# Kernel tuning notes

Hardware: AMD Instinct MI355X
Metric: run time of the kernel (lower is better)

The kernel has to match this reference:

```python
import jax, jax.numpy as jnp
import numpy as np
import math

MODEL_DIM = 1024
HEAD_DIM = 64
NUM_HEADS = 16
FF_MULT = 4
FF_DIM = FF_MULT * MODEL_DIM
ATTN_DIM = NUM_HEADS * HEAD_DIM
FUSED_DIMS = (ATTN_DIM, ATTN_DIM, ATTN_DIM, FF_DIM, FF_DIM)


def setup_inputs() -> dict:
    key = jax.random.key(0)
    k_x, k_in, k_attn, k_ff = jax.random.split(key, 4)
    B, S = 2, 2048
    inputs = jax.random.normal(k_x, (B, S, MODEL_DIM), dtype=jnp.float32)
    # LayerNorm affine params (torch defaults: weight=1, bias=0)
    ln_w = jnp.ones((MODEL_DIM,), dtype=jnp.float32)
    ln_b = jnp.zeros((MODEL_DIM,), dtype=jnp.float32)
    # Linear weights stored as [in, out] (equivalent to torch W.T)
    s_in = 1.0 / math.sqrt(MODEL_DIM)
    w_in = jax.random.uniform(k_in, (MODEL_DIM, sum(FUSED_DIMS)), jnp.float32, -s_in, s_in)
    s_a = 1.0 / math.sqrt(ATTN_DIM)
    w_attn = jax.random.uniform(k_attn, (ATTN_DIM, MODEL_DIM), jnp.float32, -s_a, s_a)
    s_f = 1.0 / math.sqrt(FF_DIM)
    w_ff = jax.random.uniform(k_ff, (FF_DIM, MODEL_DIM), jnp.float32, -s_f, s_f)
    return {"inputs": inputs, "ln_w": ln_w, "ln_b": ln_b,
            "w_in": w_in, "w_attn": w_attn, "w_ff": w_ff}


def _layer_norm(x, w, b, eps=1e-5):
    mu = jnp.mean(x, axis=-1, keepdims=True)
    var = jnp.var(x, axis=-1, keepdims=True)
    return (x - mu) * jax.lax.rsqrt(var + eps) * w + b


def reference(inputs, ln_w, ln_b, w_in, w_attn, w_ff):
    B, S, D = inputs.shape
    units = _layer_norm(inputs, ln_w, ln_b)
    proj = units @ w_in                                   # [B,S,3*A+2*F]
    splits = np.cumsum(FUSED_DIMS)[:-1]
    q, k, v, ff, ff_gate = jnp.split(proj, splits, axis=-1)
    # split heads: [B,S,H*d] -> [B,H,S,d]
    def heads(t):
        return t.reshape(B, S, NUM_HEADS, HEAD_DIM).transpose(0, 2, 1, 3)
    q, k, v = heads(q), heads(k), heads(v)
    scale = 1.0 / math.sqrt(HEAD_DIM)
    score = jnp.einsum('bhsd,bhTd->bhsT', q, k) * scale   # [B,H,S,S]
    weight = jax.nn.softmax(score, axis=-1)
    attn = jnp.einsum('bhsT,bhTd->bhsd', weight, v)       # [B,H,S,d]
    concat = attn.transpose(0, 2, 1, 3).reshape(B, S, ATTN_DIM)
    attn_out = concat @ w_attn                            # [B,S,D]
    ff_out = (ff * jax.nn.gelu(ff_gate, approximate=True)) @ w_ff
    return inputs + attn_out + ff_out
```

## Files before the change

kernel.cpp:

```cpp
#include <hip/hip_runtime.h>
#include <hip/hip_bf16.h>
#include <cstdint>
#include <cstddef>

typedef __bf16 bf16;
typedef __bf16 bf16x8 __attribute__((ext_vector_type(8)));
typedef float f32x4 __attribute__((ext_vector_type(4)));

#define MFMA16(a, b, c) __builtin_amdgcn_mfma_f32_16x16x32_bf16(a, b, c, 0, 0, 0)

#define GLOBAL_LOAD_LDS16(gptr, lptr)                                          \
  __builtin_amdgcn_global_load_lds(                                            \
      (const __attribute__((address_space(1))) void*)(gptr),                   \
      (__attribute__((address_space(3))) void*)(lptr), 16, 0, 0)

__global__ __launch_bounds__(256) void prep(const float* __restrict__ w_in,
                                            const float* __restrict__ w_attn,
                                            const float* __restrict__ w_ff,
                                            bf16* __restrict__ wt_in,
                                            bf16* __restrict__ wtcat,
                                            const float* __restrict__ x,
                                            const float* __restrict__ ln_w,
                                            const float* __restrict__ ln_b,
                                            bf16* __restrict__ xn) {
  __shared__ __align__(16) char sm[4352];
  if (blockIdx.x < 16384) {
    float(*t)[33] = (float(*)[33])sm;
    int id = blockIdx.x;
    const float* src; bf16* dst;
    int srcN, srccol0, LDO, mode, obase, goff, kcol0, ntn;
    if (id < 3072) {
      src = w_in; dst = wt_in; srcN = 11264; srccol0 = 0; LDO = 1024;
      mode = 0; obase = 0; goff = 0; kcol0 = 0; ntn = 96;
    } else if (id < 7168) {
      id -= 3072; src = w_in; dst = wt_in; srcN = 11264; srccol0 = 3072;
      LDO = 1024; mode = 1; obase = 3072; goff = 0; kcol0 = 0; ntn = 128;
    } else if (id < 11264) {
      id -= 7168; src = w_in; dst = wt_in; srcN = 11264; srccol0 = 7168;
      LDO = 1024; mode = 1; obase = 3072; goff = 64; kcol0 = 0; ntn = 128;
    } else if (id < 12288) {
      id -= 11264; src = w_attn; dst = wtcat; srcN = 1024; srccol0 = 0;
      LDO = 5120; mode = 0; obase = 0; goff = 0; kcol0 = 0; ntn = 32;
    } else {
      id -= 12288; src = w_ff; dst = wtcat; srcN = 1024; srccol0 = 0;
      LDO = 5120; mode = 0; obase = 0; goff = 0; kcol0 = 1024; ntn = 32;
    }
    const int n0 = (id % ntn) * 32, k0 = (id / ntn) * 32;
    const int tx = threadIdx.x & 31, ty = threadIdx.x >> 5;
    for (int i = ty; i < 32; i += 8)
      t[i][tx] = src[(size_t)(k0 + i) * srcN + srccol0 + n0 + tx];
    __syncthreads();
    for (int i = ty; i < 32; i += 8) {
      int n = n0 + i;
      int orow = mode ? (obase + ((n >> 6) << 7) + goff + (n & 63)) : (obase + n);
      dst[(size_t)orow * LDO + kcol0 + k0 + tx] = (bf16)t[tx][i];
    }
  } else {
    float* rs = (float*)sm;
    float* rss = rs + 256;
    const int row = blockIdx.x - 16384;
    const int tid = threadIdx.x;
    const float* xr = x + (size_t)row * 1024;
    float4 v = *(const float4*)&xr[tid * 4];
    float s = v.x + v.y + v.z + v.w;
    float ss = v.x * v.x + v.y * v.y + v.z * v.z + v.w * v.w;
    rs[tid] = s; rss[tid] = ss;
    __syncthreads();
    for (int off = 128; off > 0; off >>= 1) {
      if (tid < off) { rs[tid] += rs[tid + off]; rss[tid] += rss[tid + off]; }
      __syncthreads();
    }
    const float mean = rs[0] * (1.f / 1024.f);
    const float var = rss[0] * (1.f / 1024.f) - mean * mean;
    const float rstd = rsqrtf(var + 1e-5f);
    const float* vp = (const float*)&v;
    for (int i = 0; i < 4; i++) {
      int c = tid * 4 + i;
      xn[(size_t)row * 1024 + c] = (bf16)((vp[i] - mean) * rstd * ln_w[c] + ln_b[c]);
    }
  }
}

__global__ __launch_bounds__(256) void vtrans(const bf16* __restrict__ proj,
                                              bf16* __restrict__ vt) {
  __shared__ bf16 t[64][80];
  const int tid = threadIdx.x;
  const int s0 = blockIdx.x * 64;
  const int h = blockIdx.y, b = blockIdx.z;
  constexpr size_t LDP = 3072;
  const bf16* src = proj + (size_t)b * 2048 * LDP + 2048 + h * 64;
  {
    int s = tid >> 2, d0 = (tid & 3) * 16;
    *(bf16x8*)&t[s][d0]     = *(const bf16x8*)&src[(size_t)(s0 + s) * LDP + d0];
    *(bf16x8*)&t[s][d0 + 8] = *(const bf16x8*)&src[(size_t)(s0 + s) * LDP + d0 + 8];
  }
  __syncthreads();
  {
    int d = tid >> 2, sb = (tid & 3) * 16;
    bf16* dst = vt + ((size_t)(b * 16 + h) * 64 + d) * 2048 + s0 + sb;
    bf16x8 o0, o1;
    for (int i = 0; i < 8; i++) { o0[i] = t[sb + i][d]; o1[i] = t[sb + 8 + i][d]; }
    *(bf16x8*)&dst[0] = o0;
    *(bf16x8*)&dst[8] = o1;
  }
}

__global__ __launch_bounds__(256) void flash_attn(const bf16* __restrict__ proj,
                                                  const bf16* __restrict__ vt,
                                                  bf16* __restrict__ hcat) {
  __shared__ __align__(16) char smem[50176];
  bf16* Ks = (bf16*)smem;
  bf16* Vs = (bf16*)(smem + 16384);
  bf16* Ps = (bf16*)(smem + 32768);
  const int tid = threadIdx.x;
  const int wave = tid >> 6, lane = tid & 63;
  const int quad = lane >> 4, l16 = lane & 15;
  const int q0 = blockIdx.x * 64;
  const int h = blockIdx.y, b = blockIdx.z;
  constexpr size_t LDP = 3072;
  const bf16* Qb = proj + (size_t)b * 2048 * LDP + h * 64;
  const bf16* Kb = proj + (size_t)b * 2048 * LDP + 1024 + h * 64;
  const bf16* Vt = vt + (size_t)(b * 16 + h) * 64 * 2048;

  const int qrow = q0 + wave * 16 + l16;
  bf16x8 aq0r = *(const bf16x8*)&Qb[(size_t)qrow * LDP + quad * 8];
  bf16x8 aq1r = *(const bf16x8*)&Qb[(size_t)qrow * LDP + 32 + quad * 8];
  bf16x8 aq0, aq1;
#pragma unroll
  for (int i = 0; i < 8; i++) {
    aq0[i] = (bf16)((float)aq0r[i] * 0.125f);
    aq1[i] = (bf16)((float)aq1r[i] * 0.125f);
  }

  f32x4 O[4] = {};
  float plrow[4] = {0.f, 0.f, 0.f, 0.f};

  const int krow_ = wave * 8 + (lane >> 3);
  const int kq_ = ((lane & 7) ^ (krow_ & 7)) * 8;
  const int vrow_ = wave * 4 + (lane >> 4);
  const int vq_ = ((lane & 15) ^ (vrow_ & 15)) * 8;

  for (int j0 = 0; j0 < 2048; j0 += 128) {
#pragma unroll
    for (int p = 0; p < 4; p++) {
      int kr = p * 32 + krow_;
      GLOBAL_LOAD_LDS16(&Kb[(size_t)(j0 + kr) * LDP + kq_],
                        &Ks[kr * 64 + (lane & 7) * 8]);
      int vr = p * 16 + vrow_;
      GLOBAL_LOAD_LDS16(&Vt[(size_t)vr * 2048 + j0 + vq_],
                        &Vs[vr * 128 + (lane & 15) * 8]);
    }
    __syncthreads();

    f32x4 sa[8];
#pragma unroll
    for (int nt = 0; nt < 8; nt++) {
      int r = nt * 16 + l16;
      bf16x8 bk0 = *(const bf16x8*)&Ks[r * 64 + (quad ^ (r & 7)) * 8];
      bf16x8 bk1 = *(const bf16x8*)&Ks[r * 64 + ((quad + 4) ^ (r & 7)) * 8];
      f32x4 t = {};
      t = MFMA16(aq0, bk0, t);
      sa[nt] = MFMA16(aq1, bk1, t);
    }

    bf16* Pw = Ps + wave * (16 * 136);
#pragma unroll
    for (int r = 0; r < 4; r++) {
      bf16* pr = &Pw[(quad * 4 + r) * 136];
      float ts = 0.f;
#pragma unroll
      for (int nt = 0; nt < 8; nt++) {
        float p = __expf(sa[nt][r]);
        pr[nt * 16 + l16] = (bf16)p;
        ts += p;
      }
      plrow[r] += ts;
    }

#pragma unroll
    for (int kg = 0; kg < 4; kg++) {
      bf16x8 aP = *(const bf16x8*)&Pw[l16 * 136 + kg * 32 + quad * 8];
#pragma unroll
      for (int nb = 0; nb < 4; nb++) {
        int vrr = nb * 16 + l16;
        int vsl = ((kg * 4 + quad) ^ (vrr & 15)) * 8;
        bf16x8 bv = *(const bf16x8*)&Vs[vrr * 128 + vsl];
        O[nb] = MFMA16(aP, bv, O[nb]);
      }
    }
    __syncthreads();
  }

#pragma unroll
  for (int r = 0; r < 4; r++) {
    float ts = plrow[r];
#pragma unroll
    for (int d = 1; d < 16; d <<= 1) ts += __shfl_xor(ts, d, 64);
    float inv = 1.f / ts;
    size_t row = (size_t)b * 2048 + q0 + wave * 16 + quad * 4 + r;
#pragma unroll
    for (int nb = 0; nb < 4; nb++)
      hcat[row * 5120 + h * 64 + nb * 16 + l16] = (bf16)(O[nb][r] * inv);
  }
}

__global__ __launch_bounds__(512, 2) void gemm_proj(const bf16* __restrict__ A,
                                                    const bf16* __restrict__ Bt,
                                                    bf16* __restrict__ proj,
                                                    bf16* __restrict__ hcat) {
  constexpr int K = 1024, NT = 32;
  __shared__ __align__(16) char smem[98304];
  const int tid = threadIdx.x;
  const int wave = tid >> 6, lane = tid & 63;
  const int quad = lane >> 4, l16 = lane & 15;
  const int wm0 = (wave >> 2) * 128, wn0 = (wave & 3) * 64;
  const size_t rowA0 = (size_t)blockIdx.y * 256;
  const size_t rowB0 = (size_t)blockIdx.x * 256;
  const bf16* Ag = A + rowA0 * K;
  const bf16* Bg = Bt + rowB0 * K;

  const int srow = tid >> 2;
  const int sslot = tid & 3;
  const int rslot = (quad ^ ((l16 >> 1) & 3)) * 8;

  f32x4 acc[8][4] = {};

  auto STAGE = [&](int kt, int buf) {
    bf16* As = (bf16*)(smem + buf * 32768);
    bf16* Bs = As + 256 * 32;
    const int k0 = kt * 32;
#pragma unroll
    for (int p = 0; p < 2; p++) {
      int r = p * 128 + srow;
      int kq = (sslot ^ ((r >> 1) & 3)) * 8;
      GLOBAL_LOAD_LDS16(&Ag[(size_t)r * K + k0 + kq], &As[r * 32 + sslot * 8]);
      GLOBAL_LOAD_LDS16(&Bg[(size_t)r * K + k0 + kq], &Bs[r * 32 + sslot * 8]);
    }
  };

  STAGE(0, 0);
  STAGE(1, 1);
  asm volatile("s_waitcnt vmcnt(4)" ::: "memory");
  __builtin_amdgcn_s_barrier();
  asm volatile("" ::: "memory");

  int cbuf = 0, sbuf = 2;
#pragma unroll 1
  for (int kt = 0; kt < NT; kt++) {
    if (kt + 2 < NT) STAGE(kt + 2, sbuf);
    const bf16* As = (const bf16*)(smem + cbuf * 32768);
    const bf16* Bs = As + 256 * 32;
    bf16x8 bfr[4];
#pragma unroll
    for (int j = 0; j < 4; j++)
      bfr[j] = *(const bf16x8*)&Bs[(wn0 + j * 16 + l16) * 32 + rslot];
#pragma unroll
    for (int ih = 0; ih < 2; ih++) {
      bf16x8 af[4];
#pragma unroll
      for (int i = 0; i < 4; i++)
        af[i] = *(const bf16x8*)&As[(wm0 + (ih * 4 + i) * 16 + l16) * 32 + rslot];
      __builtin_amdgcn_s_setprio(1);
#pragma unroll
      for (int i = 0; i < 4; i++)
#pragma unroll
        for (int j = 0; j < 4; j++)
          acc[ih * 4 + i][j] = MFMA16(af[i], bfr[j], acc[ih * 4 + i][j]);
      __builtin_amdgcn_s_setprio(0);
    }
    if (kt + 2 < NT) {
      asm volatile("s_waitcnt vmcnt(4)" ::: "memory");
    } else {
      asm volatile("s_waitcnt vmcnt(0)" ::: "memory");
    }
    __builtin_amdgcn_s_barrier();
    asm volatile("" ::: "memory");
    cbuf = (cbuf == 2) ? 0 : cbuf + 1;
    sbuf = (sbuf == 2) ? 0 : sbuf + 1;
  }

  {
    const int T2 = (int)blockIdx.x - 12;
    bf16* Cs = (bf16*)smem;
    constexpr int LDC2 = 264;
#pragma unroll 1
    for (int h = 0; h < 2; h++) {
      if ((wave >> 2) == h) {
#pragma unroll
        for (int i = 0; i < 8; i++)
#pragma unroll
          for (int j = 0; j < 4; j++)
#pragma unroll
            for (int r = 0; r < 4; r++)
              Cs[(i * 16 + quad * 4 + r) * LDC2 + wn0 + j * 16 + l16] =
                  (bf16)acc[i][j][r];
      }
      __syncthreads();
      if (T2 < 0) {
#pragma unroll
        for (int it = 0; it < 8; it++) {
          int idx = it * 512 + tid;
          int row = idx >> 5, ch = (idx & 31) * 8;
          *(bf16x8*)&proj[(rowA0 + h * 128 + row) * 3072 + rowB0 + ch] =
              *(const bf16x8*)&Cs[row * LDC2 + ch];
        }
      } else {
#pragma unroll
        for (int it = 0; it < 4; it++) {
          int idx = it * 512 + tid;
          int row = idx >> 4;
          int p = (idx >> 3) & 1, c8 = (idx & 7) * 8;
          bf16x8 f = *(const bf16x8*)&Cs[row * LDC2 + p * 128 + c8];
          bf16x8 g = *(const bf16x8*)&Cs[row * LDC2 + p * 128 + 64 + c8];
          bf16x8 o;
#pragma unroll
          for (int i = 0; i < 8; i++) {
            float xg = (float)g[i];
            float u = 0.7978845608f * (xg + 0.044715f * xg * xg * xg);
            float gl = xg / (1.f + __expf(-2.f * u));
            o[i] = (bf16)((float)f[i] * gl);
          }
          *(bf16x8*)&hcat[(rowA0 + h * 128 + row) * 5120 + 1024 +
                          (2 * T2 + p) * 64 + c8] = o;
        }
      }
      __syncthreads();
    }
  }
}

__global__ __launch_bounds__(256) void gemm_out(const bf16* __restrict__ A,
                                                const bf16* __restrict__ Bt,
                                                bf16* __restrict__ part) {
  constexpr int LDAB = 5120, LDC = 136;
  __shared__ __align__(16) char smem[32768];
  bf16* As = (bf16*)smem;
  bf16* Bs = As + 128 * 64;
  bf16* Cs = (bf16*)smem;
  const int tid = threadIdx.x;
  const int wave = tid >> 6, lane = tid & 63;
  const int quad = lane >> 4, l16 = lane & 15;
  constexpr int NM = 4, NN = 4;
  const int wm0 = (wave >> 1) * 64, wn0 = (wave & 1) * 64;
  const size_t rowA0 = (size_t)blockIdx.y * 128;
  const size_t rowB0 = (size_t)blockIdx.x * 128;
  const int kbeg = blockIdx.z * 1280, kend = kbeg + 1280;

  const int srow = tid >> 3;
  const int sq = ((tid & 7) ^ (srow & 7)) * 8;
  const int sslot = (tid & 7) * 8;

  f32x4 acc[NM][NN] = {};

  for (int k0 = kbeg; k0 < kend; k0 += 64) {
#pragma unroll
    for (int p = 0; p < 4; p++) {
      int r = p * 32 + srow;
      GLOBAL_LOAD_LDS16(&A[(rowA0 + r) * LDAB + k0 + sq], &As[r * 64 + sslot]);
      GLOBAL_LOAD_LDS16(&Bt[(rowB0 + r) * LDAB + k0 + sq], &Bs[r * 64 + sslot]);
    }
    __syncthreads();
#pragma unroll
    for (int c = 0; c < 2; c++) {
      bf16x8 af[NM], bfr[NN];
#pragma unroll
      for (int i = 0; i < NM; i++) {
        int r = wm0 + i * 16 + l16;
        af[i] = *(const bf16x8*)&As[r * 64 + ((c * 4 + quad) ^ (r & 7)) * 8];
      }
#pragma unroll
      for (int j = 0; j < NN; j++) {
        int r = wn0 + j * 16 + l16;
        bfr[j] = *(const bf16x8*)&Bs[r * 64 + ((c * 4 + quad) ^ (r & 7)) * 8];
      }
#pragma unroll
      for (int i = 0; i < NM; i++)
#pragma unroll
        for (int j = 0; j < NN; j++)
          acc[i][j] = MFMA16(af[i], bfr[j], acc[i][j]);
    }
    __syncthreads();
  }

  bf16* dst = part + (size_t)blockIdx.z * (4096 * 1024);
#pragma unroll
  for (int half = 0; half < 2; half++) {
    if ((wave >> 1) == half) {
#pragma unroll
      for (int i = 0; i < NM; i++)
#pragma unroll
        for (int j = 0; j < NN; j++)
#pragma unroll
          for (int r = 0; r < 4; r++)
            Cs[(i * 16 + quad * 4 + r) * LDC + wn0 + j * 16 + l16] =
                (bf16)acc[i][j][r];
    }
    __syncthreads();
    const int c0 = (tid & 15) * 8;
#pragma unroll
    for (int it = 0; it < 4; it++) {
      int row = (tid >> 4) + it * 16;
      *(bf16x8*)&dst[(rowA0 + half * 64 + row) * 1024 + rowB0 + c0] =
          *(const bf16x8*)&Cs[row * LDC + c0];
    }
    __syncthreads();
  }
}

__global__ __launch_bounds__(256) void reduce_out(const float* __restrict__ x,
                                                  const bf16* __restrict__ part,
                                                  float* __restrict__ out) {
  const size_t i = ((size_t)blockIdx.x * 256 + threadIdx.x) * 8;
  constexpr size_t SL = 4096 * 1024;
  float r[8];
  float4 x0 = *(const float4*)&x[i];
  float4 x1 = *(const float4*)&x[i + 4];
  r[0] = x0.x; r[1] = x0.y; r[2] = x0.z; r[3] = x0.w;
  r[4] = x1.x; r[5] = x1.y; r[6] = x1.z; r[7] = x1.w;
#pragma unroll
  for (int z = 0; z < 4; z++) {
    bf16x8 p = *(const bf16x8*)&part[z * SL + i];
#pragma unroll
    for (int k = 0; k < 8; k++) r[k] += (float)p[k];
  }
  float4 o0 = {r[0], r[1], r[2], r[3]};
  float4 o1 = {r[4], r[5], r[6], r[7]};
  *(float4*)&out[i] = o0;
  *(float4*)&out[i + 4] = o1;
}

extern "C" void kernel_launch(void* const* d_in, const int* in_sizes, int n_in,
                              void* d_out, int out_size, void* d_ws, size_t ws_size,
                              hipStream_t stream) {
  const float* x      = (const float*)d_in[0];
  const float* ln_w   = (const float*)d_in[1];
  const float* ln_b   = (const float*)d_in[2];
  const float* w_in   = (const float*)d_in[3];
  const float* w_attn = (const float*)d_in[4];
  const float* w_ff   = (const float*)d_in[5];
  float* out = (float*)d_out;
  char* ws = (char*)d_ws;

  bf16* wt_in = (bf16*)(ws);
  bf16* wtcat = (bf16*)(ws + 23068672);
  bf16* xn    = (bf16*)(ws + 33554432);
  bf16* proj  = (bf16*)(ws + 41943040);
  bf16* part  = (bf16*)(ws + 67108864);
  bf16* vt    = (bf16*)(ws + 100663296);
  bf16* hcat  = (bf16*)(ws + 134217728);

  prep<<<20480, 256, 0, stream>>>(w_in, w_attn, w_ff, wt_in, wtcat,
                                  x, ln_w, ln_b, xn);
  gemm_proj<<<dim3(44, 16), 512, 0, stream>>>(xn, wt_in, proj, hcat);
  vtrans<<<dim3(32, 16, 2), 256, 0, stream>>>(proj, vt);
  flash_attn<<<dim3(32, 16, 2), 256, 0, stream>>>(proj, vt, hcat);
  gemm_out<<<dim3(8, 32, 4), 256, 0, stream>>>(hcat, wtcat, part);
  reduce_out<<<2048, 256, 0, stream>>>(x, part, out);
}
```

Baseline: 392.1 us.

## Split gemm_proj stage loads into A/B halves interleaved with MFMA phases

Splits the per-iteration global-to-LDS prefetch of the projection GEMM into separate A and B issues. Each is placed between LDS fragment reads and an MFMA half-block, with extra workgroup barriers so the waves move through the phases together. The aim is to spread memory issue across the compute and overlap loads with MFMA, in the style of a ping-pong schedule. The cost is two extra barriers per k-step, which may add sync overhead.

New measurement: 401.8 us. 1.02x slower.

```diff
diff --git a/kernel.cpp b/kernel.cpp
--- a/kernel.cpp
+++ b/kernel.cpp
@@ -208,7 +208,7 @@
                                                     const bf16* __restrict__ Bt,
                                                     bf16* __restrict__ proj,
                                                     bf16* __restrict__ hcat) {
-  constexpr int K = 1024, NT = 32;
+  constexpr int K = 1024, NKT = 32;
   __shared__ __align__(16) char smem[98304];
   const int tid = threadIdx.x;
   const int wave = tid >> 6, lane = tid & 63;
@@ -225,50 +225,73 @@
 
   f32x4 acc[8][4] = {};
 
-  auto STAGE = [&](int kt, int buf) {
+  auto STAGE_A = [&](int kt, int buf) {
     bf16* As = (bf16*)(smem + buf * 32768);
-    bf16* Bs = As + 256 * 32;
     const int k0 = kt * 32;
 #pragma unroll
     for (int p = 0; p < 2; p++) {
       int r = p * 128 + srow;
       int kq = (sslot ^ ((r >> 1) & 3)) * 8;
       GLOBAL_LOAD_LDS16(&Ag[(size_t)r * K + k0 + kq], &As[r * 32 + sslot * 8]);
+    }
+  };
+  auto STAGE_B = [&](int kt, int buf) {
+    bf16* Bs = (bf16*)(smem + buf * 32768) + 256 * 32;
+    const int k0 = kt * 32;
+#pragma unroll
+    for (int p = 0; p < 2; p++) {
+      int r = p * 128 + srow;
+      int kq = (sslot ^ ((r >> 1) & 3)) * 8;
       GLOBAL_LOAD_LDS16(&Bg[(size_t)r * K + k0 + kq], &Bs[r * 32 + sslot * 8]);
     }
   };
 
-  STAGE(0, 0);
-  STAGE(1, 1);
+  STAGE_A(0, 0); STAGE_B(0, 0);
+  STAGE_A(1, 1); STAGE_B(1, 1);
   asm volatile("s_waitcnt vmcnt(4)" ::: "memory");
   __builtin_amdgcn_s_barrier();
   asm volatile("" ::: "memory");
 
   int cbuf = 0, sbuf = 2;
 #pragma unroll 1
-  for (int kt = 0; kt < NT; kt++) {
-    if (kt + 2 < NT) STAGE(kt + 2, sbuf);
+  for (int kt = 0; kt < NKT; kt++) {
     const bf16* As = (const bf16*)(smem + cbuf * 32768);
     const bf16* Bs = As + 256 * 32;
-    bf16x8 bfr[4];
+    const bool st = (kt + 2 < NKT);
+
+    bf16x8 bfr[4], af[4];
 #pragma unroll
     for (int j = 0; j < 4; j++)
       bfr[j] = *(const bf16x8*)&Bs[(wn0 + j * 16 + l16) * 32 + rslot];
 #pragma unroll
-    for (int ih = 0; ih < 2; ih++) {
-      bf16x8 af[4];
-#pragma unroll
-      for (int i = 0; i < 4; i++)
-        af[i] = *(const bf16x8*)&As[(wm0 + (ih * 4 + i) * 16 + l16) * 32 + rslot];
-      __builtin_amdgcn_s_setprio(1);
-#pragma unroll
-      for (int i = 0; i < 4; i++)
-#pragma unroll
-        for (int j = 0; j < 4; j++)
-          acc[ih * 4 + i][j] = MFMA16(af[i], bfr[j], acc[ih * 4 + i][j]);
-      __builtin_amdgcn_s_setprio(0);
-    }
-    if (kt + 2 < NT) {
+    for (int i = 0; i < 4; i++)
+      af[i] = *(const bf16x8*)&As[(wm0 + i * 16 + l16) * 32 + rslot];
+    if (st) STAGE_A(kt + 2, sbuf);
+    __builtin_amdgcn_s_barrier();
+    asm volatile("s_waitcnt lgkmcnt(0)" ::: "memory");
+    __builtin_amdgcn_s_setprio(1);
+#pragma unroll
+    for (int i = 0; i < 4; i++)
+#pragma unroll
+      for (int j = 0; j < 4; j++)
+        acc[i][j] = MFMA16(af[i], bfr[j], acc[i][j]);
+    __builtin_amdgcn_s_setprio(0);
+    __builtin_amdgcn_s_barrier();
+
+#pragma unroll
+    for (int i = 0; i < 4; i++)
+      af[i] = *(const bf16x8*)&As[(wm0 + 64 + i * 16 + l16) * 32 + rslot];
+    if (st) STAGE_B(kt + 2, sbuf);
+    __builtin_amdgcn_s_barrier();
+    asm volatile("s_waitcnt lgkmcnt(0)" ::: "memory");
+    __builtin_amdgcn_s_setprio(1);
+#pragma unroll
+    for (int i = 0; i < 4; i++)
+#pragma unroll
+      for (int j = 0; j < 4; j++)
+        acc[4 + i][j] = MFMA16(af[i], bfr[j], acc[4 + i][j]);
+    __builtin_amdgcn_s_setprio(0);
+    if (kt < NKT - 2) {
       asm volatile("s_waitcnt vmcnt(4)" ::: "memory");
     } else {
       asm volatile("s_waitcnt vmcnt(0)" ::: "memory");
```
